# Optimization experiments

Hardware: AMD Instinct MI355X
Metric: run time of the kernel (lower is better)

Reference implementation:

```python
import jax, jax.numpy as jnp
import numpy as np

# Production-scale dims (see shape_source)
N = 100_000      # total nodes (tokens)
E = 1_600_000    # edges
B = 2_000        # graphs / documents
VOCAB = 50_000
NW = 256         # word_vec width == GraphConv out channels (args.nw)
ENC = 512        # args.enc_nh
K = 100          # args.num_topic
EPS = 1e-5       # BatchNorm eps


def setup_inputs() -> dict:
    key = jax.random.key(0)
    ks = jax.random.split(key, 24)
    idx_x = jax.random.randint(ks[0], (N,), 0, VOCAB)
    idx_w = jnp.ones((1,), jnp.float32)          # scalar self-loop weight
    x_batch = jnp.sort(jax.random.randint(ks[1], (N,), 0, B))
    edge_index = jax.random.randint(ks[2], (2, E), 0, N)
    edge_weight = jax.random.uniform(ks[3], (E,), jnp.float32)
    # Parameters
    s = 0.02
    word_vec = jax.random.normal(ks[4], (VOCAB, NW), jnp.float32) * s
    Wrel = jax.random.normal(ks[5], (NW, NW), jnp.float32) * s   # GraphConv lin_rel
    brel = jnp.zeros((NW,), jnp.float32)
    Wroot = jax.random.normal(ks[6], (NW, NW), jnp.float32) * s  # GraphConv lin_root (no bias)
    bn_gamma = jnp.ones((NW,), jnp.float32)
    bn_beta = jnp.zeros((NW,), jnp.float32)
    W1 = jax.random.normal(ks[7], (ENC, 2 * NW), jnp.float32) * s  # enc2_fc1
    b1 = jnp.zeros((ENC,), jnp.float32)
    W2 = jax.random.normal(ks[8], (ENC, 2 * NW), jnp.float32) * s  # enc2_fc2
    b2 = jnp.zeros((ENC,), jnp.float32)
    Wm = jax.random.normal(ks[9], (K, ENC), jnp.float32) * s       # mean_fc
    bm = jnp.zeros((K,), jnp.float32)
    Wv = jnp.zeros((K, ENC), jnp.float32)                          # logvar_fc zero-init
    bv = jnp.zeros((K,), jnp.float32)
    Wphi = jax.random.normal(ks[10], (K, 2 * NW + ENC), jnp.float32) * s  # phi_fc
    bphi = jnp.zeros((K,), jnp.float32)
    return dict(idx_x=idx_x, idx_w=idx_w, x_batch=x_batch, edge_index=edge_index,
                edge_weight=edge_weight, word_vec=word_vec, Wrel=Wrel, brel=brel,
                Wroot=Wroot, bn_gamma=bn_gamma, bn_beta=bn_beta, W1=W1, b1=b1,
                W2=W2, b2=b2, Wm=Wm, bm=bm, Wv=Wv, bv=bv, Wphi=Wphi, bphi=bphi)


def reference(idx_x, idx_w, x_batch, edge_index, edge_weight, word_vec,
              Wrel, brel, Wroot, bn_gamma, bn_beta, W1, b1, W2, b2,
              Wm, bm, Wv, bv, Wphi, bphi):
    # Embedding gather
    x = word_vec[idx_x]                                # [N, NW]
    src, dst = edge_index[0], edge_index[1]
    # GraphConv with explicit self-loops of weight idx_w (diag edges in original)
    msg = edge_weight[:, None] * x[src]                # [E, NW]
    aggr = jax.ops.segment_sum(msg, dst, num_segments=N) + idx_w * x
    h = aggr @ Wrel.T + brel + x @ Wroot.T             # lin_rel(aggr) + lin_root(x)
    # BatchNorm1d (training-mode batch stats, biased variance) + tanh
    mu = jnp.mean(h, axis=0)
    var = jnp.mean((h - mu) ** 2, axis=0)
    enc1 = jnp.tanh((h - mu) * jax.lax.rsqrt(var + EPS) * bn_gamma + bn_beta)
    enc1 = jnp.concatenate([enc1, x], axis=-1)         # [N, 2*NW]
    # GLU gate
    enc2 = jax.nn.sigmoid(enc1 @ W1.T + b1) * jnp.tanh(enc1 @ W2.T + b2)  # [N, ENC]
    # Scatter-sum pooling per document (dropout is identity in eval)
    pooled = jax.ops.segment_sum(enc2, x_batch, num_segments=B)            # [B, ENC]
    mean = pooled @ Wm.T + bm                          # [B, K]
    logvar = pooled @ Wv.T + bv                        # [B, K]
    # Gather re-expansion + softmax
    word_embed = jnp.concatenate([enc1, pooled[x_batch]], axis=-1)         # [N, 2*NW+ENC]
    phi = jax.nn.softmax(word_embed @ Wphi.T + bphi, axis=-1)              # [N, K]
    return mean, logvar, phi
```

## Files before the change

kernel.cpp:

```cpp
#include <hip/hip_runtime.h>
#include <hip/hip_bf16.h>

#define NW 256
#define D2 512
#define PK 1024
#define BM 128
#define BK 64
#define DPB 8
#define SCHUNK 1024

typedef unsigned short u16;
typedef short bf16x8 __attribute__((ext_vector_type(8)));
typedef float f32x4 __attribute__((ext_vector_type(4)));

__device__ __forceinline__ float bf2f(u16 u) {
    union { unsigned u; float f; } v; v.u = ((unsigned)u) << 16; return v.f;
}
__device__ __forceinline__ u16 f2bf(float f) {
    union { float f; unsigned u; } v; v.f = f;
    unsigned u = v.u;
    return (u16)((u + 0x7fffu + ((u >> 16) & 1u)) >> 16);
}
__device__ __forceinline__ float tanh_fast(float x) {
    return 1.f - 2.f / (1.f + __expf(2.f * x));
}

__device__ __forceinline__ void stage_tile(const u16* __restrict__ base, int row0, int maxrow,
                                           int ldk, int k0, u16* lds, int tid) {
    int w = tid >> 6, l = tid & 63;
#pragma unroll
    for (int i = 0; i < 4; ++i) {
        int loadIdx = i * 256 + w * 64 + l;
        int row = loadIdx >> 3, s = loadIdx & 7;
        int srow = row0 + row; if (srow > maxrow) srow = maxrow;
        int scol = k0 + ((s ^ (row & 7)) << 3);
        const u16* g = base + (size_t)srow * ldk + scol;
        u16* ld = lds + (size_t)(i * 256 + w * 64) * 8;
        __builtin_amdgcn_global_load_lds((const __attribute__((address_space(1))) void*)g,
                                         (__attribute__((address_space(3))) void*)ld, 16, 0, 0);
    }
}

__device__ __forceinline__ bf16x8 lds_frag(const u16* lds, int row, int kc, int g) {
    int byte = (row << 7) + (kc << 6) + (g << 4);
    byte ^= (row & 7) << 4;
    return *(const bf16x8*)((const char*)lds + byte);
}

__device__ __forceinline__ void stage32(const u16* __restrict__ base, int row0, int maxrow,
                                        int ldk, int k0, u16* lds, int tid) {
    int w = tid >> 6, l = tid & 63;
#pragma unroll
    for (int i = 0; i < 2; ++i) {
        int loadIdx = i * 256 + w * 64 + l;
        int line = loadIdx >> 3, sp = loadIdx & 7;
        int slot = sp ^ (line & 3);
        int row = line * 2 + (slot >> 2);
        int g = slot & 3;
        int srow = row0 + row; if (srow > maxrow) srow = maxrow;
        int scol = k0 + g * 8;
        const u16* gp = base + (size_t)srow * ldk + scol;
        u16* ld = lds + (size_t)(i * 256 + w * 64) * 8;
        __builtin_amdgcn_global_load_lds((const __attribute__((address_space(1))) void*)gp,
                                         (__attribute__((address_space(3))) void*)ld, 16, 0, 0);
    }
}
__device__ __forceinline__ bf16x8 lds_frag32(const u16* lds, int row, int g) {
    int line = row >> 1;
    int slot = ((row & 1) << 2) + g;
    int byte = line * 128 + ((slot ^ (line & 3)) << 4);
    return *(const bf16x8*)((const char*)lds + byte);
}

__global__ void k_wprep(const float* __restrict__ Wrel, const float* __restrict__ Wroot,
                        const float* __restrict__ W1, const float* __restrict__ W2,
                        const float* __restrict__ Wphi,
                        u16* __restrict__ wcat, u16* __restrict__ wglu,
                        u16* __restrict__ wphib, float* __restrict__ sums,
                        float* __restrict__ sumsq, int K) {
    int i = blockIdx.x * blockDim.x + threadIdx.x;
    if (i < NW * D2) {
        int c = i >> 9, k = i & 511;
        float v = (k < NW) ? Wrel[c * NW + k] : Wroot[c * NW + (k - NW)];
        wcat[i] = f2bf(v);
    }
    if (i < 1024 * 512) {
        int row = i >> 9, k = i & 511;
        int c = row >> 7, j = row & 127;
        int sub = j >> 5, jj = j & 31;
        int half = sub & 1, colgrp = sub >> 1;
        int col = c * 64 + colgrp * 32 + jj;
        float v = half ? W2[(size_t)col * D2 + k] : W1[(size_t)col * D2 + k];
        wglu[i] = f2bf(v);
    }
    if (i < 128 * 1024) {
        int r = i >> 10, k = i & 1023;
        wphib[i] = f2bf(r < K ? Wphi[(size_t)r * PK + k] : 0.f);
    }
    if (i < NW) { sums[i] = 0.f; sumsq[i] = 0.f; }
}

__global__ void k_gather(const int* __restrict__ idx, const float* __restrict__ wv,
                         u16* __restrict__ X, int N) {
    int row = blockIdx.x * 4 + (threadIdx.x >> 6);
    int lane = threadIdx.x & 63;
    if (row < N) {
        int id = idx[row];
        float4 v = *(const float4*)(wv + (size_t)id * NW + lane * 4);
        ushort4 o;
        o.x = f2bf(v.x); o.y = f2bf(v.y); o.z = f2bf(v.z); o.w = f2bf(v.w);
        *(ushort4*)(X + (size_t)row * D2 + NW + lane * 4) = o;
    }
}

__global__ void k_hist(const int* __restrict__ ei, int* __restrict__ deg, int E) {
    int e = blockIdx.x * blockDim.x + threadIdx.x;
    if (e < E) atomicAdd(&deg[ei[E + e]], 1);
}
__global__ __launch_bounds__(256) void k_scan1(const int* __restrict__ deg,
                                               int* __restrict__ bsum, int N) {
    int b = blockIdx.x, t = threadIdx.x;
    int base = b * SCHUNK;
    int s = 0;
#pragma unroll
    for (int j = 0; j < SCHUNK / 256; ++j) {
        int idx = base + j * 256 + t;
        if (idx < N) s += deg[idx];
    }
    __shared__ int ls[256];
    ls[t] = s; __syncthreads();
    for (int d = 128; d > 0; d >>= 1) {
        if (t < d) ls[t] += ls[t + d];
        __syncthreads();
    }
    if (t == 0) bsum[b] = ls[0];
}
__global__ __launch_bounds__(256) void k_scan2(int* __restrict__ bsum,
                                               int* __restrict__ rowptr, int NB, int N) {
    int t = threadIdx.x;
    int v = (t < NB) ? bsum[t] : 0;
    __shared__ int ls[256];
    ls[t] = v; __syncthreads();
    for (int d = 1; d < 256; d <<= 1) {
        int x = (t >= d) ? ls[t - d] : 0;
        __syncthreads();
        ls[t] += x;
        __syncthreads();
    }
    if (t < NB) bsum[t] = ls[t] - v;
    if (t == 255) rowptr[N] = ls[255];
}
__global__ __launch_bounds__(256) void k_scan3(int* __restrict__ deg,
                                               const int* __restrict__ bsum,
                                               int* __restrict__ rowptr, int N) {
    int b = blockIdx.x, t = threadIdx.x;
    int tbase = b * SCHUNK + t * 4;
    int loc[4];
    int s = 0;
#pragma unroll
    for (int j = 0; j < 4; ++j) {
        int idx = tbase + j;
        loc[j] = (idx < N) ? deg[idx] : 0;
        s += loc[j];
    }
    __shared__ int ls[256];
    ls[t] = s; __syncthreads();
    for (int d = 1; d < 256; d <<= 1) {
        int x = (t >= d) ? ls[t - d] : 0;
        __syncthreads();
        ls[t] += x;
        __syncthreads();
    }
    int run = bsum[b] + ls[t] - s;
#pragma unroll
    for (int j = 0; j < 4; ++j) {
        int idx = tbase + j;
        if (idx < N) { rowptr[idx] = run; run += loc[j]; deg[idx] = 0; }
    }
}
__global__ void k_scatter(const int* __restrict__ ei, const float* __restrict__ ew,
                          const int* __restrict__ rowptr, int* __restrict__ cursor,
                          int* __restrict__ ecols, float* __restrict__ evals, int E) {
    int e = blockIdx.x * blockDim.x + threadIdx.x;
    if (e < E) {
        int d = ei[E + e];
        int p = rowptr[d] + atomicAdd(&cursor[d], 1);
        ecols[p] = ei[e];
        evals[p] = ew[e];
    }
}

__global__ void k_spmm(const int* __restrict__ rowptr, const int* __restrict__ ecols,
                       const float* __restrict__ evals, const float* __restrict__ idxw,
                       u16* __restrict__ X, int N) {
    int n = blockIdx.x * 4 + (threadIdx.x >> 6);
    int l = threadIdx.x & 63;
    if (n >= N) return;
    int half = l >> 5, li = l & 31;
    float a[8];
    bf16x8 xv = *(const bf16x8*)(X + (size_t)n * D2 + NW + li * 8);
    float iw = idxw[0];
#pragma unroll
    for (int j = 0; j < 8; ++j) a[j] = half ? 0.f : iw * bf2f((u16)xv[j]);
    int r0 = rowptr[n], r1 = rowptr[n + 1];
#pragma unroll 4
    for (int e = r0 + half; e < r1; e += 2) {
        int s = ecols[e];
        float w = evals[e];
        bf16x8 v = *(const bf16x8*)(X + (size_t)s * D2 + NW + li * 8);
#pragma unroll
        for (int j = 0; j < 8; ++j) a[j] += w * bf2f((u16)v[j]);
    }
#pragma unroll
    for (int j = 0; j < 8; ++j) a[j] += __shfl_xor(a[j], 32);
    if (half == 0) {
        bf16x8 o;
#pragma unroll
        for (int j = 0; j < 8; ++j) o[j] = (short)f2bf(a[j]);
        *(bf16x8*)(X + (size_t)n * D2 + li * 8) = o;
    }
}

__global__ __launch_bounds__(256) void k_gemm_h(const u16* __restrict__ A, const u16* __restrict__ W,
                                                const float* __restrict__ brel, u16* __restrict__ H,
                                                float* __restrict__ sums, float* __restrict__ sumsq,
                                                int M, int MT) {
    int b = blockIdx.x;
    int xcd = b & 7, j = b >> 3;
    int chunk = j & 1;
    int panel = (j >> 1) * 8 + xcd;
    if (panel >= MT) return;
    __shared__ u16 As[2][BM * BK], Ws[2][BM * BK];
    int tid = threadIdx.x;
    int w = tid >> 6, l = tid & 63, l16 = l & 15, g = l >> 4;
    int wr = w >> 1, wc = w & 1;
    int row0 = panel * BM;
    const u16* wbase = W + (size_t)chunk * 128 * D2;
    f32x4 acc[4][4];
#pragma unroll
    for (int m = 0; m < 4; ++m)
#pragma unroll
        for (int n = 0; n < 4; ++n) { f32x4 z = {0.f, 0.f, 0.f, 0.f}; acc[m][n] = z; }

    stage_tile(A, row0, M - 1, D2, 0, As[0], tid);
    stage_tile(wbase, 0, 127, D2, 0, Ws[0], tid);
    __syncthreads();
    int buf = 0;
    for (int kt = 0; kt < 8; ++kt) {
        if (kt < 7) {
            stage_tile(A, row0, M - 1, D2, (kt + 1) * BK, As[buf ^ 1], tid);
            stage_tile(wbase, 0, 127, D2, (kt + 1) * BK, Ws[buf ^ 1], tid);
        }
#pragma unroll
        for (int kc = 0; kc < 2; ++kc) {
            bf16x8 af[4], bfr[4];
#pragma unroll
            for (int m = 0; m < 4; ++m) af[m] = lds_frag(As[buf], wr * 64 + m * 16 + l16, kc, g);
#pragma unroll
            for (int n = 0; n < 4; ++n) bfr[n] = lds_frag(Ws[buf], wc * 64 + n * 16 + l16, kc, g);
#pragma unroll
            for (int n = 0; n < 4; ++n)
#pragma unroll
                for (int m = 0; m < 4; ++m)
                    acc[m][n] = __builtin_amdgcn_mfma_f32_16x16x32_bf16(af[m], bfr[n], acc[m][n], 0, 0, 0);
        }
        __syncthreads();
        buf ^= 1;
    }
    float* ssum = (float*)As[0];
    float* ssq  = ssum + 128;
    if (tid < 128) { ssum[tid] = 0.f; ssq[tid] = 0.f; }
    __syncthreads();
    int colb = chunk * 128;
#pragma unroll
    for (int n = 0; n < 4; ++n) {
        int lcol = wc * 64 + n * 16 + l16;
        int col = colb + lcol;
        float bb = brel[col];
        float cs = 0.f, cq = 0.f;
#pragma unroll
        for (int m = 0; m < 4; ++m) {
            int row = row0 + wr * 64 + m * 16 + g * 4;
#pragma unroll
            for (int r = 0; r < 4; ++r) {
                if (row + r < M) {
                    float v = acc[m][n][r] + bb;
                    H[(size_t)(row + r) * NW + col] = f2bf(v);
                    cs += v; cq += v * v;
                }
            }
        }
        cs += __shfl_xor(cs, 16); cs += __shfl_xor(cs, 32);
        cq += __shfl_xor(cq, 16); cq += __shfl_xor(cq, 32);
        if (g == 0) { atomicAdd(&ssum[lcol], cs); atomicAdd(&ssq[lcol], cq); }
    }
    __syncthreads();
    if (tid < 128) {
        atomicAdd(&sums[colb + tid], ssum[tid]);
        atomicAdd(&sumsq[colb + tid], ssq[tid]);
    }
}

__global__ void k_bnprep(const float* __restrict__ sums, const float* __restrict__ sumsq,
                         const float* __restrict__ gamma, const float* __restrict__ beta,
                         float* __restrict__ bnab, int N) {
    int c = threadIdx.x;
    float inv = 1.f / (float)N;
    float mu = sums[c] * inv;
    float var = sumsq[c] * inv - mu * mu;
    float rs = rsqrtf(var + 1e-5f);
    float a = rs * gamma[c];
    bnab[c] = a;
    bnab[NW + c] = beta[c] - mu * a;
}

__global__ void k_enc1(const u16* __restrict__ H, const float* __restrict__ bnab,
                       u16* __restrict__ X, int N) {
    int row = blockIdx.x * 4 + (threadIdx.x >> 6);
    int lane = threadIdx.x & 63;
    if (row >= N) return;
    int c = lane * 4;
    ushort4 hv = *(const ushort4*)(H + (size_t)row * NW + c);
    ushort4 o;
    o.x = f2bf(tanh_fast(bf2f(hv.x) * bnab[c + 0] + bnab[NW + c + 0]));
    o.y = f2bf(tanh_fast(bf2f(hv.y) * bnab[c + 1] + bnab[NW + c + 1]));
    o.z = f2bf(tanh_fast(bf2f(hv.z) * bnab[c + 2] + bnab[NW + c + 2]));
    o.w = f2bf(tanh_fast(bf2f(hv.w) * bnab[c + 3] + bnab[NW + c + 3]));
    *(ushort4*)(X + (size_t)row * D2 + c) = o;
}

__global__ __launch_bounds__(256) void k_glu(const u16* __restrict__ A, const u16* __restrict__ Wp,
                                             const float* __restrict__ b1, const float* __restrict__ b2,
                                             u16* __restrict__ enc2, int M, int MT) {
    int b = blockIdx.x;
    int xcd = b & 7, j = b >> 3;
    int chunk = j & 7;
    int panel = (j >> 3) * 8 + xcd;
    if (panel >= MT) return;
    __shared__ u16 As[2][BM * 32], Ws[2][BM * 32];
    int tid = threadIdx.x;
    int w = tid >> 6, l = tid & 63, l16 = l & 15, g = l >> 4;
    int wr = w >> 1, wc = w & 1;
    int row0 = panel * BM;
    const u16* wbase = Wp + (size_t)chunk * 128 * D2;
    f32x4 acc[4][4];
#pragma unroll
    for (int m = 0; m < 4; ++m)
#pragma unroll
        for (int n = 0; n < 4; ++n) { f32x4 z = {0.f, 0.f, 0.f, 0.f}; acc[m][n] = z; }

    stage32(A, row0, M - 1, D2, 0, As[0], tid);
    stage32(wbase, 0, 127, D2, 0, Ws[0], tid);
    __syncthreads();
    int buf = 0;
    for (int kt = 0; kt < 16; ++kt) {
        if (kt < 15) {
            stage32(A, row0, M - 1, D2, (kt + 1) * 32, As[buf ^ 1], tid);
            stage32(wbase, 0, 127, D2, (kt + 1) * 32, Ws[buf ^ 1], tid);
        }
        {
            bf16x8 af[4], bfr[4];
#pragma unroll
            for (int m = 0; m < 4; ++m) af[m] = lds_frag32(As[buf], wr * 64 + m * 16 + l16, g);
#pragma unroll
            for (int n = 0; n < 4; ++n) bfr[n] = lds_frag32(Ws[buf], wc * 64 + n * 16 + l16, g);
#pragma unroll
            for (int n = 0; n < 4; ++n)
#pragma unroll
                for (int m = 0; m < 4; ++m)
                    acc[m][n] = __builtin_amdgcn_mfma_f32_16x16x32_bf16(af[m], bfr[n], acc[m][n], 0, 0, 0);
        }
        __syncthreads();
        buf ^= 1;
    }
    int colb = chunk * 64 + wc * 32;
#pragma unroll
    for (int n = 0; n < 2; ++n) {
        int col = colb + n * 16 + l16;
        float f1 = b1[col], f2 = b2[col];
#pragma unroll
        for (int m = 0; m < 4; ++m) {
            int row = row0 + wr * 64 + m * 16 + g * 4;
#pragma unroll
            for (int r = 0; r < 4; ++r) {
                if (row + r < M) {
                    float g1 = acc[m][n][r] + f1;
                    float g2 = acc[m][n + 2][r] + f2;
                    float sg = 1.f / (1.f + __expf(-g1));
                    enc2[(size_t)(row + r) * D2 + col] = f2bf(sg * tanh_fast(g2));
                }
            }
        }
    }
}

__global__ void k_docptr(const int* __restrict__ xb, int* __restrict__ dp, int N, int B) {
    int b = blockIdx.x * blockDim.x + threadIdx.x;
    if (b <= B) {
        int lo = 0, hi = N;
        while (lo < hi) { int mid = (lo + hi) >> 1; if (xb[mid] < b) lo = mid + 1; else hi = mid; }
        dp[b] = lo;
    }
}

__global__ void k_pool(const u16* __restrict__ enc2, const int* __restrict__ dp,
                       float* __restrict__ pooled, u16* __restrict__ pooledb, int B) {
    int b = blockIdx.x, t = threadIdx.x;
    int r0 = dp[b], r1 = dp[b + 1];
    float a0 = 0.f, a1 = 0.f;
    for (int r = r0; r < r1; ++r) {
        a0 += bf2f(enc2[(size_t)r * D2 + t]);
        a1 += bf2f(enc2[(size_t)r * D2 + 256 + t]);
    }
    pooled[(size_t)b * D2 + t] = a0;
    pooled[(size_t)b * D2 + 256 + t] = a1;
    pooledb[(size_t)b * D2 + t] = f2bf(a0);
    pooledb[(size_t)b * D2 + 256 + t] = f2bf(a1);
}

__global__ __launch_bounds__(128) void k_meanvar(const float* __restrict__ pooled,
                                                 const float* __restrict__ Wm,
                                                 const float* __restrict__ bm,
                                                 const float* __restrict__ Wv,
                                                 const float* __restrict__ bv,
                                                 float* __restrict__ out, int B, int K) {
    __shared__ float sp[DPB][D2];
    int b0 = blockIdx.x * DPB;
    int t = threadIdx.x;
    for (int i = t; i < DPB * D2; i += 128) {
        int d = i >> 9, c = i & 511;
        int b = b0 + d;
        sp[d][c] = (b < B) ? pooled[(size_t)b * D2 + c] : 0.f;
    }
    __syncthreads();
    if (t < K) {
        float m[DPB], v[DPB];
#pragma unroll
        for (int d = 0; d < DPB; ++d) { m[d] = 0.f; v[d] = 0.f; }
        const float* wm = Wm + (size_t)t * D2;
        const float* wv = Wv + (size_t)t * D2;
        for (int c = 0; c < D2; ++c) {
            float a = wm[c], bb = wv[c];
#pragma unroll
            for (int d = 0; d < DPB; ++d) {
                m[d] += sp[d][c] * a;
                v[d] += sp[d][c] * bb;
            }
        }
        float mb = bm[t], vb = bv[t];
#pragma unroll
        for (int d = 0; d < DPB; ++d) {
            int b = b0 + d;
            if (b < B) {
                out[(size_t)b * K + t] = m[d] + mb;
                out[(size_t)B * K + (size_t)b * K + t] = v[d] + vb;
            }
        }
    }
}

__device__ __forceinline__ void stage_phiA(const u16* __restrict__ X, const u16* __restrict__ PB,
                                           const int* __restrict__ xb, int row0, int M,
                                           int k0, u16* lds, int tid) {
    int w = tid >> 6, l = tid & 63;
#pragma unroll
    for (int i = 0; i < 4; ++i) {
        int loadIdx = i * 256 + w * 64 + l;
        int row = loadIdx >> 3, s = loadIdx & 7;
        int srow = row0 + row; if (srow >= M) srow = M - 1;
        int scol = k0 + ((s ^ (row & 7)) << 3);
        const u16* gsrc = (scol < D2) ? X + (size_t)srow * D2 + scol
                                      : PB + (size_t)xb[srow] * D2 + (scol - D2);
        u16* ld = lds + (size_t)(i * 256 + w * 64) * 8;
        __builtin_amdgcn_global_load_lds((const __attribute__((address_space(1))) void*)gsrc,
                                         (__attribute__((address_space(3))) void*)ld, 16, 0, 0);
    }
}

__global__ __launch_bounds__(256) void k_phi(const u16* __restrict__ X, const u16* __restrict__ PB,
                                             const int* __restrict__ xb, const u16* __restrict__ Wp,
                                             const float* __restrict__ bphi, float* __restrict__ out,
                                             int M, int B, int K) {
    __shared__ u16 As[2][BM * BK], Ws[2][BM * BK];
    int tid = threadIdx.x;
    int w = tid >> 6, l = tid & 63, l16 = l & 15, g = l >> 4;
    int row0 = blockIdx.x * BM;
    f32x4 acc[2][8];
#pragma unroll
    for (int m = 0; m < 2; ++m)
#pragma unroll
        for (int n = 0; n < 8; ++n) { f32x4 z = {0.f, 0.f, 0.f, 0.f}; acc[m][n] = z; }

    stage_phiA(X, PB, xb, row0, M, 0, As[0], tid);
    stage_tile(Wp, 0, 127, PK, 0, Ws[0], tid);
    __syncthreads();
    int buf = 0;
    for (int kt = 0; kt < 16; ++kt) {
        if (kt < 15) {
            stage_phiA(X, PB, xb, row0, M, (kt + 1) * BK, As[buf ^ 1], tid);
            stage_tile(Wp, 0, 127, PK, (kt + 1) * BK, Ws[buf ^ 1], tid);
        }
#pragma unroll
        for (int kc = 0; kc < 2; ++kc) {
            bf16x8 a0 = lds_frag(As[buf], w * 32 + l16, kc, g);
            bf16x8 a1 = lds_frag(As[buf], w * 32 + 16 + l16, kc, g);
#pragma unroll
            for (int n = 0; n < 8; ++n) {
                bf16x8 bb = lds_frag(Ws[buf], n * 16 + l16, kc, g);
                acc[0][n] = __builtin_amdgcn_mfma_f32_16x16x32_bf16(a0, bb, acc[0][n], 0, 0, 0);
                acc[1][n] = __builtin_amdgcn_mfma_f32_16x16x32_bf16(a1, bb, acc[1][n], 0, 0, 0);
            }
        }
        __syncthreads();
        buf ^= 1;
    }
    size_t outoff = (size_t)2 * B * K;
#pragma unroll
    for (int m = 0; m < 2; ++m) {
        int rb = row0 + w * 32 + m * 16 + g * 4;
#pragma unroll
        for (int r = 0; r < 4; ++r) {
            int row = rb + r;
            if (row >= M) continue;
            float v[7];
            float mx = -1e30f;
#pragma unroll
            for (int n = 0; n < 7; ++n) {
                int col = n * 16 + l16;
                float t = (col < K) ? acc[m][n][r] + bphi[col] : -1e30f;
                v[n] = t;
                mx = fmaxf(mx, t);
            }
            mx = fmaxf(mx, __shfl_xor(mx, 1));
            mx = fmaxf(mx, __shfl_xor(mx, 2));
            mx = fmaxf(mx, __shfl_xor(mx, 4));
            mx = fmaxf(mx, __shfl_xor(mx, 8));
            float s = 0.f;
#pragma unroll
            for (int n = 0; n < 7; ++n) {
                int col = n * 16 + l16;
                float e = (col < K) ? __expf(v[n] - mx) : 0.f;
                v[n] = e;
                s += e;
            }
            s += __shfl_xor(s, 1);
            s += __shfl_xor(s, 2);
            s += __shfl_xor(s, 4);
            s += __shfl_xor(s, 8);
            float inv = 1.f / s;
#pragma unroll
            for (int n = 0; n < 7; ++n) {
                int col = n * 16 + l16;
                if (col < K) out[outoff + (size_t)row * K + col] = v[n] * inv;
            }
        }
    }
}

extern "C" void kernel_launch(void* const* d_in, const int* in_sizes, int n_in,
                              void* d_out, int out_size, void* d_ws, size_t ws_size,
                              hipStream_t stream) {
    const int N = in_sizes[0];
    const int E = in_sizes[4];
    const int K = in_sizes[16];
    const int B = (int)(((size_t)out_size - (size_t)N * K) / (2 * (size_t)K));

    const int*   idx_x   = (const int*)d_in[0];
    const float* idx_w   = (const float*)d_in[1];
    const int*   x_batch = (const int*)d_in[2];
    const int*   ei      = (const int*)d_in[3];
    const float* ew      = (const float*)d_in[4];
    const float* word_vec= (const float*)d_in[5];
    const float* Wrel    = (const float*)d_in[6];
    const float* brel    = (const float*)d_in[7];
    const float* Wroot   = (const float*)d_in[8];
    const float* gamma   = (const float*)d_in[9];
    const float* beta    = (const float*)d_in[10];
    const float* W1      = (const float*)d_in[11];
    const float* b1      = (const float*)d_in[12];
    const float* W2      = (const float*)d_in[13];
    const float* b2      = (const float*)d_in[14];
    const float* Wm      = (const float*)d_in[15];
    const float* bm      = (const float*)d_in[16];
    const float* Wv      = (const float*)d_in[17];
    const float* bv      = (const float*)d_in[18];
    const float* Wphi    = (const float*)d_in[19];
    const float* bphi    = (const float*)d_in[20];
    float* out = (float*)d_out;

    char* p = (char*)d_ws;
    auto take = [&](size_t bytes) -> char* {
        char* r = p;
        p += (bytes + 255) & ~(size_t)255;
        return r;
    };
    u16* X = (u16*)take((size_t)N * D2 * 2);
    char* Ybase = take((size_t)N * D2 * 2);
    u16*   hb   = (u16*)Ybase;
    u16*   enc2 = (u16*)Ybase;
    char* q = Ybase;
    auto takeY = [&](size_t bytes) -> char* {
        char* r = q;
        q += (bytes + 255) & ~(size_t)255;
        return r;
    };
    int*   rowptr = (int*)takeY((size_t)(N + 1) * 4);
    int*   cursor = (int*)takeY((size_t)N * 4);
    int*   ecols  = (int*)takeY((size_t)E * 4);
    float* evals  = (float*)takeY((size_t)E * 4);
    u16*   wcat    = (u16*)take((size_t)NW * D2 * 2);
    u16*   wglu    = (u16*)take((size_t)1024 * D2 * 2);
    u16*   wphib   = (u16*)take((size_t)128 * PK * 2);
    int*   docptr  = (int*)take((size_t)(B + 1) * 4);
    float* pooled  = (float*)take((size_t)B * D2 * 4);
    u16*   pooledb = (u16*)take((size_t)B * D2 * 2);
    float* sums    = (float*)take(NW * 4);
    float* sumsq   = (float*)take(NW * 4);
    float* bnab    = (float*)take(2 * NW * 4);
    int*   bsum    = (int*)take(256 * 4);

    if ((size_t)(p - (char*)d_ws) > ws_size) return;

    hipMemsetAsync(cursor, 0, (size_t)N * 4, stream);

    k_wprep<<<(1024 * 512 + 255) / 256, 256, 0, stream>>>(Wrel, Wroot, W1, W2, Wphi,
                                                          wcat, wglu, wphib, sums, sumsq, K);

    k_gather<<<(N + 3) / 4, 256, 0, stream>>>(idx_x, word_vec, X, N);
    k_hist<<<(E + 255) / 256, 256, 0, stream>>>(ei, cursor, E);
    int NB = (N + SCHUNK - 1) / SCHUNK;
    k_scan1<<<NB, 256, 0, stream>>>(cursor, bsum, N);
    k_scan2<<<1, 256, 0, stream>>>(bsum, rowptr, NB, N);
    k_scan3<<<NB, 256, 0, stream>>>(cursor, bsum, rowptr, N);
    k_scatter<<<(E + 255) / 256, 256, 0, stream>>>(ei, ew, rowptr, cursor, ecols, evals, E);
    k_spmm<<<(N + 3) / 4, 256, 0, stream>>>(rowptr, ecols, evals, idx_w, X, N);

    int MT = (N + BM - 1) / BM;
    int P8 = (MT + 7) / 8;
    k_gemm_h<<<P8 * 8 * 2, 256, 0, stream>>>(X, wcat, brel, hb, sums, sumsq, N, MT);
    k_bnprep<<<1, NW, 0, stream>>>(sums, sumsq, gamma, beta, bnab, N);
    k_enc1<<<(N + 3) / 4, 256, 0, stream>>>(hb, bnab, X, N);

    k_glu<<<P8 * 8 * 8, 256, 0, stream>>>(X, wglu, b1, b2, enc2, N, MT);

    k_docptr<<<(B + 1 + 255) / 256, 256, 0, stream>>>(x_batch, docptr, N, B);
    k_pool<<<B, 256, 0, stream>>>(enc2, docptr, pooled, pooledb, B);
    k_meanvar<<<(B + DPB - 1) / DPB, 128, 0, stream>>>(pooled, Wm, bm, Wv, bv, out, B, K);
    k_phi<<<MT, 256, 0, stream>>>(X, pooledb, x_batch, wphib, bphi, out, N, B, K);
}
```

Measured before the change: 764.2 us.

## Fuse BN prep and docptr into consumers, shrink GEMM tiles, trim phi columns

BatchNorm coefficient computation moves into k_enc1, where each block recomputes them into shared memory, and the doc-range binary search moves into k_pool. This removes two tiny kernel launches. k_gemm_h switches from 64-wide to 32-wide K tiles, halving its LDS footprint, and the spmm loop unroll rises to 8. k_phi drops the eighth 16-column MFMA tile because K=100 fits in 112 columns. The fused kernels repeat small per-block work, and the narrower K tiles double the number of barriers in k_gemm_h.

After: 767.9 us. No clear change (+0.5%).

```diff
diff --git a/kernel.cpp b/kernel.cpp
--- a/kernel.cpp
+++ b/kernel.cpp
@@ -203,7 +203,7 @@
 #pragma unroll
     for (int j = 0; j < 8; ++j) a[j] = half ? 0.f : iw * bf2f((u16)xv[j]);
     int r0 = rowptr[n], r1 = rowptr[n + 1];
-#pragma unroll 4
+#pragma unroll 8
     for (int e = r0 + half; e < r1; e += 2) {
         int s = ecols[e];
         float w = evals[e];
@@ -230,7 +230,7 @@
     int chunk = j & 1;
     int panel = (j >> 1) * 8 + xcd;
     if (panel >= MT) return;
-    __shared__ u16 As[2][BM * BK], Ws[2][BM * BK];
+    __shared__ u16 As[2][BM * 32], Ws[2][BM * 32];
     int tid = threadIdx.x;
     int w = tid >> 6, l = tid & 63, l16 = l & 15, g = l >> 4;
     int wr = w >> 1, wc = w & 1;
@@ -242,22 +242,21 @@
 #pragma unroll
         for (int n = 0; n < 4; ++n) { f32x4 z = {0.f, 0.f, 0.f, 0.f}; acc[m][n] = z; }
 
-    stage_tile(A, row0, M - 1, D2, 0, As[0], tid);
-    stage_tile(wbase, 0, 127, D2, 0, Ws[0], tid);
+    stage32(A, row0, M - 1, D2, 0, As[0], tid);
+    stage32(wbase, 0, 127, D2, 0, Ws[0], tid);
     __syncthreads();
     int buf = 0;
-    for (int kt = 0; kt < 8; ++kt) {
-        if (kt < 7) {
-            stage_tile(A, row0, M - 1, D2, (kt + 1) * BK, As[buf ^ 1], tid);
-            stage_tile(wbase, 0, 127, D2, (kt + 1) * BK, Ws[buf ^ 1], tid);
-        }
-#pragma unroll
-        for (int kc = 0; kc < 2; ++kc) {
+    for (int kt = 0; kt < 16; ++kt) {
+        if (kt < 15) {
+            stage32(A, row0, M - 1, D2, (kt + 1) * 32, As[buf ^ 1], tid);
+            stage32(wbase, 0, 127, D2, (kt + 1) * 32, Ws[buf ^ 1], tid);
+        }
+        {
             bf16x8 af[4], bfr[4];
 #pragma unroll
-            for (int m = 0; m < 4; ++m) af[m] = lds_frag(As[buf], wr * 64 + m * 16 + l16, kc, g);
-#pragma unroll
-            for (int n = 0; n < 4; ++n) bfr[n] = lds_frag(Ws[buf], wc * 64 + n * 16 + l16, kc, g);
+            for (int m = 0; m < 4; ++m) af[m] = lds_frag32(As[buf], wr * 64 + m * 16 + l16, g);
+#pragma unroll
+            for (int n = 0; n < 4; ++n) bfr[n] = lds_frag32(Ws[buf], wc * 64 + n * 16 + l16, g);
 #pragma unroll
             for (int n = 0; n < 4; ++n)
 #pragma unroll
@@ -301,31 +300,34 @@
     }
 }
 
-__global__ void k_bnprep(const float* __restrict__ sums, const float* __restrict__ sumsq,
-                         const float* __restrict__ gamma, const float* __restrict__ beta,
-                         float* __restrict__ bnab, int N) {
-    int c = threadIdx.x;
-    float inv = 1.f / (float)N;
-    float mu = sums[c] * inv;
-    float var = sumsq[c] * inv - mu * mu;
-    float rs = rsqrtf(var + 1e-5f);
-    float a = rs * gamma[c];
-    bnab[c] = a;
-    bnab[NW + c] = beta[c] - mu * a;
-}
-
-__global__ void k_enc1(const u16* __restrict__ H, const float* __restrict__ bnab,
-                       u16* __restrict__ X, int N) {
-    int row = blockIdx.x * 4 + (threadIdx.x >> 6);
-    int lane = threadIdx.x & 63;
+__global__ __launch_bounds__(256) void k_enc1(const u16* __restrict__ H,
+                                              const float* __restrict__ sums,
+                                              const float* __restrict__ sumsq,
+                                              const float* __restrict__ gamma,
+                                              const float* __restrict__ beta,
+                                              u16* __restrict__ X, int N) {
+    __shared__ float sa[NW], sb[NW];
+    int tid = threadIdx.x;
+    {
+        float inv = 1.f / (float)N;
+        float mu = sums[tid] * inv;
+        float var = sumsq[tid] * inv - mu * mu;
+        float rs = rsqrtf(var + 1e-5f);
+        float a = rs * gamma[tid];
+        sa[tid] = a;
+        sb[tid] = beta[tid] - mu * a;
+    }
+    __syncthreads();
+    int row = blockIdx.x * 4 + (tid >> 6);
+    int lane = tid & 63;
     if (row >= N) return;
     int c = lane * 4;
     ushort4 hv = *(const ushort4*)(H + (size_t)row * NW + c);
     ushort4 o;
-    o.x = f2bf(tanh_fast(bf2f(hv.x) * bnab[c + 0] + bnab[NW + c + 0]));
-    o.y = f2bf(tanh_fast(bf2f(hv.y) * bnab[c + 1] + bnab[NW + c + 1]));
-    o.z = f2bf(tanh_fast(bf2f(hv.z) * bnab[c + 2] + bnab[NW + c + 2]));
-    o.w = f2bf(tanh_fast(bf2f(hv.w) * bnab[c + 3] + bnab[NW + c + 3]));
+    o.x = f2bf(tanh_fast(bf2f(hv.x) * sa[c + 0] + sb[c + 0]));
+    o.y = f2bf(tanh_fast(bf2f(hv.y) * sa[c + 1] + sb[c + 1]));
+    o.z = f2bf(tanh_fast(bf2f(hv.z) * sa[c + 2] + sb[c + 2]));
+    o.w = f2bf(tanh_fast(bf2f(hv.w) * sa[c + 3] + sb[c + 3]));
     *(ushort4*)(X + (size_t)row * D2 + c) = o;
 }
 
@@ -394,19 +396,18 @@
     }
 }
 
-__global__ void k_docptr(const int* __restrict__ xb, int* __restrict__ dp, int N, int B) {
-    int b = blockIdx.x * blockDim.x + threadIdx.x;
-    if (b <= B) {
+__global__ void k_pool(const u16* __restrict__ enc2, const int* __restrict__ xb,
+                       float* __restrict__ pooled, u16* __restrict__ pooledb, int B, int N) {
+    __shared__ int rng[2];
+    int b = blockIdx.x, t = threadIdx.x;
+    if (t < 2) {
+        int target = b + t;
         int lo = 0, hi = N;
-        while (lo < hi) { int mid = (lo + hi) >> 1; if (xb[mid] < b) lo = mid + 1; else hi = mid; }
-        dp[b] = lo;
-    }
-}
-
-__global__ void k_pool(const u16* __restrict__ enc2, const int* __restrict__ dp,
-                       float* __restrict__ pooled, u16* __restrict__ pooledb, int B) {
-    int b = blockIdx.x, t = threadIdx.x;
-    int r0 = dp[b], r1 = dp[b + 1];
+        while (lo < hi) { int mid = (lo + hi) >> 1; if (xb[mid] < target) lo = mid + 1; else hi = mid; }
+        rng[t] = lo;
+    }
+    __syncthreads();
+    int r0 = rng[0], r1 = rng[1];
     float a0 = 0.f, a1 = 0.f;
     for (int r = r0; r < r1; ++r) {
         a0 += bf2f(enc2[(size_t)r * D2 + t]);
@@ -485,11 +486,11 @@
     int tid = threadIdx.x;
     int w = tid >> 6, l = tid & 63, l16 = l & 15, g = l >> 4;
     int row0 = blockIdx.x * BM;
-    f32x4 acc[2][8];
+    f32x4 acc[2][7];
 #pragma unroll
     for (int m = 0; m < 2; ++m)
 #pragma unroll
-        for (int n = 0; n < 8; ++n) { f32x4 z = {0.f, 0.f, 0.f, 0.f}; acc[m][n] = z; }
+        for (int n = 0; n < 7; ++n) { f32x4 z = {0.f, 0.f, 0.f, 0.f}; acc[m][n] = z; }
 
     stage_phiA(X, PB, xb, row0, M, 0, As[0], tid);
     stage_tile(Wp, 0, 127, PK, 0, Ws[0], tid);
@@ -505,7 +506,7 @@
             bf16x8 a0 = lds_frag(As[buf], w * 32 + l16, kc, g);
             bf16x8 a1 = lds_frag(As[buf], w * 32 + 16 + l16, kc, g);
 #pragma unroll
-            for (int n = 0; n < 8; ++n) {
+            for (int n = 0; n < 7; ++n) {
                 bf16x8 bb = lds_frag(Ws[buf], n * 16 + l16, kc, g);
                 acc[0][n] = __builtin_amdgcn_mfma_f32_16x16x32_bf16(a0, bb, acc[0][n], 0, 0, 0);
                 acc[1][n] = __builtin_amdgcn_mfma_f32_16x16x32_bf16(a1, bb, acc[1][n], 0, 0, 0);
@@ -611,12 +612,10 @@
     u16*   wcat    = (u16*)take((size_t)NW * D2 * 2);
     u16*   wglu    = (u16*)take((size_t)1024 * D2 * 2);
     u16*   wphib   = (u16*)take((size_t)128 * PK * 2);
-    int*   docptr  = (int*)take((size_t)(B + 1) * 4);
     float* pooled  = (float*)take((size_t)B * D2 * 4);
     u16*   pooledb = (u16*)take((size_t)B * D2 * 2);
     float* sums    = (float*)take(NW * 4);
     float* sumsq   = (float*)take(NW * 4);
-    float* bnab    = (float*)take(2 * NW * 4);
     int*   bsum    = (int*)take(256 * 4);
 
     if ((size_t)(p - (char*)d_ws) > ws_size) return;
@@ -638,13 +637,11 @@
     int MT = (N + BM - 1) / BM;
     int P8 = (MT + 7) / 8;
     k_gemm_h<<<P8 * 8 * 2, 256, 0, stream>>>(X, wcat, brel, hb, sums, sumsq, N, MT);
-    k_bnprep<<<1, NW, 0, stream>>>(sums, sumsq, gamma, beta, bnab, N);
-    k_enc1<<<(N + 3) / 4, 256, 0, stream>>>(hb, bnab, X, N);
+    k_enc1<<<(N + 3) / 4, 256, 0, stream>>>(hb, sums, sumsq, gamma, beta, X, N);
 
     k_glu<<<P8 * 8 * 8, 256, 0, stream>>>(X, wglu, b1, b2, enc2, N, MT);
 
-    k_docptr<<<(B + 1 + 255) / 256, 256, 0, stream>>>(x_batch, docptr, N, B);
-    k_pool<<<B, 256, 0, stream>>>(enc2, docptr, pooled, pooledb, B);
+    k_pool<<<B, 256, 0, stream>>>(enc2, x_batch, pooled, pooledb, B, N);
     k_meanvar<<<(B + DPB - 1) / DPB, 128, 0, stream>>>(pooled, Wm, bm, Wv, bv, out, B, K);
     k_phi<<<MT, 256, 0, stream>>>(X, pooledb, x_batch, wphib, bphi, out, N, B, K);
 }
```
